# Kernel optimization log

Measured on AMD Instinct MI355X. Metric: run time of the kernel, lower is better.

Reference implementation:

```python
import jax
import jax.numpy as jnp
import numpy as np
from jax import lax

IOU_THRESH = 0.5
TOP, LEFT, BOTTOM, RIGHT = 0, 1, 2, 3


def setup_inputs() -> dict:
    key = jax.random.key(0)
    k1, k2, k3, k4, k5 = jax.random.split(key, 5)
    B, N, C = 4, 3000, 21
    # plausible boxes in (top, left, bottom, right) with positive height/width
    tl = jax.random.uniform(k1, (B, N, 2), dtype=jnp.float32) * 800.0
    wh = jax.random.uniform(k2, (B, N, 2), dtype=jnp.float32) * 200.0 + 1.0
    nms_reg = jnp.concatenate([tl, tl + wh], axis=2)
    nms_cls = jax.random.normal(k3, (B, N, 1), dtype=jnp.float32)
    rcnn_reg = jax.random.normal(k4, (B, N, 4), dtype=jnp.float32) * 2.0
    rcnn_cls = jax.random.normal(k5, (B, N, C), dtype=jnp.float32)
    return {"nms_reg": nms_reg, "nms_cls": nms_cls,
            "rcnn_reg": rcnn_reg, "rcnn_cls": rcnn_cls, "reduction": 16}


def _pairwise_iou(boxes):
    # boxes: [N, 4] in (top, left, bottom, right). IoU is invariant to the
    # (x, y) axis permutation the original applies before torchvision.nms.
    t, l, b, r = boxes[:, 0], boxes[:, 1], boxes[:, 2], boxes[:, 3]
    area = jnp.maximum(b - t, 0.0) * jnp.maximum(r - l, 0.0)  # [N]
    ih = jnp.maximum(jnp.minimum(b[:, None], b[None, :]) - jnp.maximum(t[:, None], t[None, :]), 0.0)
    iw = jnp.maximum(jnp.minimum(r[:, None], r[None, :]) - jnp.maximum(l[:, None], l[None, :]), 0.0)
    inter = ih * iw  # [N, N]
    union = area[:, None] + area[None, :] - inter
    return inter / jnp.maximum(union, 1e-9)


def _nms_keep(iou, scores):
    # Greedy NMS over one class. iou: [N, N]; scores: [N] (-inf = not this class).
    # Matches torchvision.ops.nms: suppress boxes with IoU > threshold.
    N = scores.shape[0]
    idx = jnp.arange(N)

    def step(state, _):
        rem, keep = state
        i = jnp.argmax(rem)
        valid = rem[i] > -jnp.inf
        keep = keep.at[i].set(valid)
        suppress = (iou[i] > IOU_THRESH) | (idx == i)
        rem = jnp.where(valid & suppress, -jnp.inf, rem)
        return (rem, keep), None

    (_, keep), _ = lax.scan(step, (scores, jnp.zeros(N, dtype=bool)), None, length=N)
    return keep


def reference(nms_reg, nms_cls, rcnn_reg, rcnn_cls, reduction):
    red = jnp.float32(reduction)
    # round top/left down, bottom/right up on the feature grid, back to pixels
    nms_reg_rounded = jnp.concatenate(
        [jnp.floor(nms_reg[:, :, :2] * red), jnp.ceil(nms_reg[:, :, 2:] * red)],
        axis=2) / red
    # rcnn_reg[:, :, c] += nms_reg_rounded[:, :, c] for all 4 coords
    boxes = rcnn_reg + nms_reg_rounded  # [B, N, 4]
    probs = jax.nn.softmax(rcnn_cls, axis=2)  # [B, N, C]
    nms_cls_sig = jax.nn.sigmoid(nms_cls)

    amax = jnp.argmax(probs, axis=2)  # [B, N]
    C = probs.shape[2]
    class_ids = jnp.arange(1, C)  # skip background class 0
    # per-class masked scores: [B, C-1, N]
    cls_scores = jnp.transpose(probs, (0, 2, 1))[:, 1:, :]
    scores = jnp.where(amax[:, None, :] == class_ids[None, :, None],
                       cls_scores, -jnp.inf)

    iou = jax.vmap(_pairwise_iou)(boxes)  # [B, N, N] (shared across classes)
    keep_per_class = jax.vmap(lambda io, sc: jax.vmap(lambda s: _nms_keep(io, s))(sc))(iou, scores)  # [B, C-1, N]
    keep = jnp.any(keep_per_class, axis=1)  # [B, N]; argmax classes are disjoint

    return (nms_reg_rounded, nms_cls_sig, boxes, probs, keep)
```

## Files before the change

### kernel.cpp

```cpp
#include <hip/hip_runtime.h>
#include <cfloat>
#include <climits>

#define B 4
#define N 3000
#define C 21
#define SORT_N 256
#define WORDS 4
#define NMS_BLOCKS (B * (C - 1))
#define PW_BLOCKS 12
#define TPB 1024


__device__ __forceinline__ int softmax_am(const float* __restrict__ lg,
                                          float* __restrict__ pmax_out,
                                          float* __restrict__ pstore) {
    float m = lg[0];
    #pragma unroll
    for (int c = 1; c < C; ++c) m = fmaxf(m, lg[c]);
    float p[C];
    float sum = 0.0f;
    #pragma unroll
    for (int c = 0; c < C; ++c) {
        p[c] = expf(__fsub_rn(lg[c], m));
        sum = __fadd_rn(sum, p[c]);
    }
    float best = -1.0f; int bc = 0;
    #pragma unroll
    for (int c = 0; c < C; ++c) {
        float pc = __fdiv_rn(p[c], sum);
        if (pstore) pstore[c] = pc;
        if (pc > best) { best = pc; bc = c; }
    }
    *pmax_out = best;
    return bc;
}

__device__ __forceinline__ void make_boxes(float4 nr, float4 rr, float red,
                                           float4* rounded, float4* box) {
    float r0 = floorf(__fmul_rn(nr.x, red)) / red;
    float r1 = floorf(__fmul_rn(nr.y, red)) / red;
    float r2 = ceilf (__fmul_rn(nr.z, red)) / red;
    float r3 = ceilf (__fmul_rn(nr.w, red)) / red;
    *rounded = make_float4(r0, r1, r2, r3);
    *box = make_float4(__fadd_rn(rr.x, r0), __fadd_rn(rr.y, r1),
                       __fadd_rn(rr.z, r2), __fadd_rn(rr.w, r3));
}

__global__ __launch_bounds__(TPB) void fused_kernel(
    const float* __restrict__ nms_reg,
    const float* __restrict__ nms_cls,
    const float* __restrict__ rcnn_reg,
    const float* __restrict__ rcnn_cls,
    const int* __restrict__ red_p,
    float* __restrict__ out)
{
    const int tid = threadIdx.x;

    float* out_round = out;
    float* out_sig   = out + B * N * 4;
    float* out_boxes = out + B * N * 5;
    float* out_probs = out + B * N * 9;
    float* out_keep  = out + B * N * 30;

    if (blockIdx.x >= NMS_BLOCKS) {
        const int bn = (blockIdx.x - NMS_BLOCKS) * TPB + tid;
        if (bn >= B * N) return;

        float red = (float)(*red_p);

        float4 nr = ((const float4*)nms_reg)[bn];
        float4 rr = ((const float4*)rcnn_reg)[bn];
        float4 rounded, box;
        make_boxes(nr, rr, red, &rounded, &box);
        ((float4*)out_round)[bn] = rounded;
        ((float4*)out_boxes)[bn] = box;

        float x = nms_cls[bn];
        float s;
        if (x >= 0.0f) s = 1.0f / (1.0f + expf(-x));
        else { float e = expf(x); s = e / (1.0f + e); }
        out_sig[bn] = s;

        float pm;
        int am = softmax_am(rcnn_cls + (size_t)bn * C, &pm, out_probs + (size_t)bn * C);

        if (am == 0) out_keep[bn] = 0.0f;
        return;
    }

    const int b = blockIdx.x / (C - 1);
    const int c = blockIdx.x % (C - 1) + 1;
    const int lane = tid & 63;

    __shared__ int   gid[SORT_N];
    __shared__ float gsc[SORT_N];
    __shared__ int   rnk[SORT_N];
    __shared__ int   sid[SORT_N];
    __shared__ float bt[SORT_N], bl[SORT_N], bb[SORT_N], br_[SORT_N], ar[SORT_N];
    __shared__ __align__(16) unsigned long long msk[SORT_N][WORDS];
    __shared__ unsigned long long aout[WORDS];
    __shared__ int mcount;

    if (tid == 0) mcount = 0;
    if (tid < SORT_N) rnk[tid] = 0;
    __syncthreads();

    #pragma unroll
    for (int chunk = 0; chunk < 3; ++chunk) {
        int n = chunk * TPB + tid;
        bool match = false;
        float pm = 0.0f;
        if (n < N) {
            int am = softmax_am(rcnn_cls + (size_t)(b * N + n) * C, &pm, nullptr);
            match = (am == c);
        }
        unsigned long long mb = __ballot(match);
        int base = 0;
        if (lane == 0 && mb) base = atomicAdd(&mcount, __popcll(mb));
        base = __shfl(base, 0);
        if (match) {
            int pos = base + __popcll(mb & ((1ull << lane) - 1ull));
            if (pos < SORT_N) { gid[pos] = n; gsc[pos] = pm; }
        }
    }
    __syncthreads();
    const int M = min(mcount, SORT_N);

    {
        int e = tid & 255, q = tid >> 8;
        if (e < M) {
            float mys = gsc[e]; int myi = gid[e];
            int j0 = q * 64, j1 = min(j0 + 64, M);
            int partial = 0;
            for (int j = j0; j < j1; ++j) {
                float sj = gsc[j]; int ij = gid[j];
                partial += ((sj > mys) || (sj == mys && ij < myi)) ? 1 : 0;
            }
            if (partial) atomicAdd(&rnk[e], partial);
        }
    }
    __syncthreads();

    if (tid < M) {
        float red = (float)(*red_p);
        int n = gid[tid];
        int rank = rnk[tid];
        float4 nr = ((const float4*)nms_reg)[b * N + n];
        float4 rr = ((const float4*)rcnn_reg)[b * N + n];
        float4 rounded, box;
        make_boxes(nr, rr, red, &rounded, &box);
        sid[rank] = n;
        bt[rank] = box.x; bl[rank] = box.y; bb[rank] = box.z; br_[rank] = box.w;
        ar[rank] = __fmul_rn(fmaxf(__fsub_rn(box.z, box.x), 0.0f),
                             fmaxf(__fsub_rn(box.w, box.y), 0.0f));
    }
    __syncthreads();

    {
        int g = tid >> 8;
        int j = tid & 255;
        int w = (tid >> 6) & 3;
        float jt = 0.f, jl = 0.f, jb = 0.f, jr = 0.f, ja = 0.f;
        if (j < M) { jt = bt[j]; jl = bl[j]; jb = bb[j]; jr = br_[j]; ja = ar[j]; }
        int r0 = g * 64, r1 = min(r0 + 64, M);
        const double THR = 0.5 + 0x1p-25;
        for (int r = r0; r < r1; ++r) {
            float rt = bt[r], rl = bl[r], rb = bb[r], rr2 = br_[r], ra = ar[r];
            bool supp = false;
            if (j > r && j < M) {
                float ih = fmaxf(__fsub_rn(fminf(rb, jb), fmaxf(rt, jt)), 0.0f);
                float iw = fmaxf(__fsub_rn(fminf(rr2, jr), fmaxf(rl, jl)), 0.0f);
                float inter = __fmul_rn(ih, iw);
                float uni = __fsub_rn(__fadd_rn(ra, ja), inter);
                float den = fmaxf(uni, 1e-9f);
                supp = ((double)inter > (double)den * THR);
            }
            unsigned long long wm = __ballot(supp);
            if (lane == 0) msk[r][w] = wm;
        }
    }
    __syncthreads();

    if (tid < 64) {
        auto onesk = [](int k) -> unsigned long long {
            return k <= 0 ? 0ull : (k >= 64 ? ~0ull : ((1ull << k) - 1ull));
        };
        unsigned long long a0 = onesk(M), a1 = onesk(M - 64), a2 = onesk(M - 128), a3 = onesk(M - 192);
        {
            int e = min(64, M);
            #pragma unroll 4
            for (int i = 0; i < e; ++i) {
                unsigned long long sel = 0ull - ((a0 >> i) & 1ull);
                a0 &= ~(msk[i][0] & sel);
                a1 &= ~(msk[i][1] & sel);
                a2 &= ~(msk[i][2] & sel);
                a3 &= ~(msk[i][3] & sel);
            }
        }
        {
            int e = min(128, M);
            #pragma unroll 4
            for (int i = 64; i < e; ++i) {
                unsigned long long sel = 0ull - ((a1 >> (i - 64)) & 1ull);
                a1 &= ~(msk[i][1] & sel);
                a2 &= ~(msk[i][2] & sel);
                a3 &= ~(msk[i][3] & sel);
            }
        }
        {
            int e = min(192, M);
            #pragma unroll 4
            for (int i = 128; i < e; ++i) {
                unsigned long long sel = 0ull - ((a2 >> (i - 128)) & 1ull);
                a2 &= ~(msk[i][2] & sel);
                a3 &= ~(msk[i][3] & sel);
            }
        }
        {
            int e = min(256, M);
            #pragma unroll 4
            for (int i = 192; i < e; ++i) {
                unsigned long long sel = 0ull - ((a3 >> (i - 192)) & 1ull);
                a3 &= ~(msk[i][3] & sel);
            }
        }
        if (lane == 0) { aout[0] = a0; aout[1] = a1; aout[2] = a2; aout[3] = a3; }
    }
    __syncthreads();

    if (tid < M) {
        unsigned long long aw = aout[tid >> 6];
        bool kept = (aw >> (tid & 63)) & 1ull;
        int n = sid[tid];
        out_keep[b * N + n] = (kept && n != 0) ? 1.0f : 0.0f;
    }
}

extern "C" void kernel_launch(void* const* d_in, const int* in_sizes, int n_in,
                              void* d_out, int out_size, void* d_ws, size_t ws_size,
                              hipStream_t stream) {
    const float* nms_reg  = (const float*)d_in[0];
    const float* nms_cls  = (const float*)d_in[1];
    const float* rcnn_reg = (const float*)d_in[2];
    const float* rcnn_cls = (const float*)d_in[3];
    const int*   red_p    = (const int*)d_in[4];
    float* out = (float*)d_out;

    dim3 grid(NMS_BLOCKS + PW_BLOCKS);
    fused_kernel<<<grid, TPB, 0, stream>>>(nms_reg, nms_cls, rcnn_reg, rcnn_cls, red_p, out);
}
```

Measured before the change: 102.1 us.

## Stage class logits through shared memory tiles with coalesced loads in NMS blocks

Each NMS block now copies the batch's rcnn_cls logits into a padded shared-memory tile with coalesced global reads, then computes softmax and argmax from shared memory instead of making strided per-thread row reads. The argmax is taken on unnormalised exponentials and the max probability becomes 1/sum, with an exact-division fallback when several exponentials are close to the maximum. The staging buffer is reused for the box arrays and suppression mask to keep the shared-memory footprint down. In exchange, only 500 of 1024 threads do compute per tile, and the extra barriers serialise load and compute across six tiles.

```diff
diff --git a/kernel.cpp b/kernel.cpp
--- a/kernel.cpp
+++ b/kernel.cpp
@@ -10,31 +10,10 @@
 #define NMS_BLOCKS (B * (C - 1))
 #define PW_BLOCKS 12
 #define TPB 1024
-
-
-__device__ __forceinline__ int softmax_am(const float* __restrict__ lg,
-                                          float* __restrict__ pmax_out,
-                                          float* __restrict__ pstore) {
-    float m = lg[0];
-    #pragma unroll
-    for (int c = 1; c < C; ++c) m = fmaxf(m, lg[c]);
-    float p[C];
-    float sum = 0.0f;
-    #pragma unroll
-    for (int c = 0; c < C; ++c) {
-        p[c] = expf(__fsub_rn(lg[c], m));
-        sum = __fadd_rn(sum, p[c]);
-    }
-    float best = -1.0f; int bc = 0;
-    #pragma unroll
-    for (int c = 0; c < C; ++c) {
-        float pc = __fdiv_rn(p[c], sum);
-        if (pstore) pstore[c] = pc;
-        if (pc > best) { best = pc; bc = c; }
-    }
-    *pmax_out = best;
-    return bc;
-}
+#define TILE_ROWS 500
+#define NTILES 6
+#define ROW_PITCH 23
+
 
 __device__ __forceinline__ void make_boxes(float4 nr, float4 rr, float red,
                                            float4* rounded, float4* box) {
@@ -82,38 +61,95 @@
         else { float e = expf(x); s = e / (1.0f + e); }
         out_sig[bn] = s;
 
-        float pm;
-        int am = softmax_am(rcnn_cls + (size_t)bn * C, &pm, out_probs + (size_t)bn * C);
-
+        const float* lg = rcnn_cls + (size_t)bn * C;
+        float m = lg[0];
+        #pragma unroll
+        for (int cc = 1; cc < C; ++cc) m = fmaxf(m, lg[cc]);
+        float p[C];
+        float sum = 0.0f;
+        #pragma unroll
+        for (int cc = 0; cc < C; ++cc) {
+            p[cc] = expf(__fsub_rn(lg[cc], m));
+            sum = __fadd_rn(sum, p[cc]);
+        }
+        float* po = out_probs + (size_t)bn * C;
+        float best = -1.0f; int am = 0;
+        #pragma unroll
+        for (int cc = 0; cc < C; ++cc) {
+            float pc = __fdiv_rn(p[cc], sum);
+            po[cc] = pc;
+            if (pc > best) { best = pc; am = cc; }
+        }
         if (am == 0) out_keep[bn] = 0.0f;
         return;
     }
 
     const int b = blockIdx.x / (C - 1);
-    const int c = blockIdx.x % (C - 1) + 1;
+    const int cblk = blockIdx.x % (C - 1) + 1;
     const int lane = tid & 63;
 
     __shared__ int   gid[SORT_N];
     __shared__ float gsc[SORT_N];
     __shared__ int   rnk[SORT_N];
     __shared__ int   sid[SORT_N];
-    __shared__ float bt[SORT_N], bl[SORT_N], bb[SORT_N], br_[SORT_N], ar[SORT_N];
-    __shared__ __align__(16) unsigned long long msk[SORT_N][WORDS];
     __shared__ unsigned long long aout[WORDS];
     __shared__ int mcount;
+    __shared__ __align__(16) char ubuf[TILE_ROWS * ROW_PITCH * 4];
+    float* stage = (float*)ubuf;
+    float* bt  = (float*)ubuf;
+    float* bl  = bt + SORT_N;
+    float* bb  = bl + SORT_N;
+    float* br_ = bb + SORT_N;
+    float* ar  = br_ + SORT_N;
+    unsigned long long* msk = (unsigned long long*)(ubuf + 5 * SORT_N * 4);
 
     if (tid == 0) mcount = 0;
     if (tid < SORT_N) rnk[tid] = 0;
     __syncthreads();
 
-    #pragma unroll
-    for (int chunk = 0; chunk < 3; ++chunk) {
-        int n = chunk * TPB + tid;
-        bool match = false;
-        float pm = 0.0f;
-        if (n < N) {
-            int am = softmax_am(rcnn_cls + (size_t)(b * N + n) * C, &pm, nullptr);
-            match = (am == c);
+    for (int t = 0; t < NTILES; ++t) {
+        const float* gsrc = rcnn_cls + ((size_t)b * N + t * TILE_ROWS) * C;
+        for (int w = tid; w < TILE_ROWS * C; w += TPB) {
+            int r = w / C;
+            int col = w - r * C;
+            stage[r * ROW_PITCH + col] = gsrc[w];
+        }
+        __syncthreads();
+
+        bool match = false; float score = 0.0f; int nrow = 0;
+        if (tid < TILE_ROWS) {
+            const float* row = stage + tid * ROW_PITCH;
+            float lgv[C];
+            #pragma unroll
+            for (int cc = 0; cc < C; ++cc) lgv[cc] = row[cc];
+            float m = lgv[0];
+            #pragma unroll
+            for (int cc = 1; cc < C; ++cc) m = fmaxf(m, lgv[cc]);
+            float p[C];
+            float sum = 0.0f;
+            float pm = -1.0f; int am = 0;
+            #pragma unroll
+            for (int cc = 0; cc < C; ++cc) {
+                p[cc] = expf(__fsub_rn(lgv[cc], m));
+                sum = __fadd_rn(sum, p[cc]);
+                if (p[cc] > pm) { pm = p[cc]; am = cc; }
+            }
+            int near = 0;
+            #pragma unroll
+            for (int cc = 0; cc < C; ++cc) near += (p[cc] >= 0.9999995f) ? 1 : 0;
+            if (near > 1) {
+                float best = -1.0f; am = 0;
+                #pragma unroll
+                for (int cc = 0; cc < C; ++cc) {
+                    float pc = __fdiv_rn(p[cc], sum);
+                    if (pc > best) { best = pc; am = cc; }
+                }
+                score = best;
+            } else {
+                score = __fdiv_rn(1.0f, sum);
+            }
+            match = (am == cblk);
+            nrow = t * TILE_ROWS + tid;
         }
         unsigned long long mb = __ballot(match);
         int base = 0;
@@ -121,10 +157,10 @@
         base = __shfl(base, 0);
         if (match) {
             int pos = base + __popcll(mb & ((1ull << lane) - 1ull));
-            if (pos < SORT_N) { gid[pos] = n; gsc[pos] = pm; }
-        }
-    }
-    __syncthreads();
+            if (pos < SORT_N) { gid[pos] = nrow; gsc[pos] = score; }
+        }
+        __syncthreads();
+    }
     const int M = min(mcount, SORT_N);
 
     {
@@ -177,7 +213,7 @@
                 supp = ((double)inter > (double)den * THR);
             }
             unsigned long long wm = __ballot(supp);
-            if (lane == 0) msk[r][w] = wm;
+            if (lane == 0) msk[(r << 2) | w] = wm;
         }
     }
     __syncthreads();
@@ -192,10 +228,10 @@
             #pragma unroll 4
             for (int i = 0; i < e; ++i) {
                 unsigned long long sel = 0ull - ((a0 >> i) & 1ull);
-                a0 &= ~(msk[i][0] & sel);
-                a1 &= ~(msk[i][1] & sel);
-                a2 &= ~(msk[i][2] & sel);
-                a3 &= ~(msk[i][3] & sel);
+                a0 &= ~(msk[(i << 2) | 0] & sel);
+                a1 &= ~(msk[(i << 2) | 1] & sel);
+                a2 &= ~(msk[(i << 2) | 2] & sel);
+                a3 &= ~(msk[(i << 2) | 3] & sel);
             }
         }
         {
@@ -203,9 +239,9 @@
             #pragma unroll 4
             for (int i = 64; i < e; ++i) {
                 unsigned long long sel = 0ull - ((a1 >> (i - 64)) & 1ull);
-                a1 &= ~(msk[i][1] & sel);
-                a2 &= ~(msk[i][2] & sel);
-                a3 &= ~(msk[i][3] & sel);
+                a1 &= ~(msk[(i << 2) | 1] & sel);
+                a2 &= ~(msk[(i << 2) | 2] & sel);
+                a3 &= ~(msk[(i << 2) | 3] & sel);
             }
         }
         {
@@ -213,8 +249,8 @@
             #pragma unroll 4
             for (int i = 128; i < e; ++i) {
                 unsigned long long sel = 0ull - ((a2 >> (i - 128)) & 1ull);
-                a2 &= ~(msk[i][2] & sel);
-                a3 &= ~(msk[i][3] & sel);
+                a2 &= ~(msk[(i << 2) | 2] & sel);
+                a3 &= ~(msk[(i << 2) | 3] & sel);
             }
         }
         {
@@ -222,7 +258,7 @@
             #pragma unroll 4
             for (int i = 192; i < e; ++i) {
                 unsigned long long sel = 0ull - ((a3 >> (i - 192)) & 1ull);
-                a3 &= ~(msk[i][3] & sel);
+                a3 &= ~(msk[(i << 2) | 3] & sel);
             }
         }
         if (lane == 0) { aout[0] = a0; aout[1] = a1; aout[2] = a2; aout[3] = a3; }
```

Result: slower. 116.8 us (+14.3%).

## Stage softmax rows through LDS for coalesced loads/stores across more blocks

Applied to the files above, without the earlier changes.

The pointwise blocks now load each group of 69 rows of logits into shared memory with coalesced reads, run the softmax per row from LDS, write probabilities back to LDS, then store them coalesced to global memory. The pointwise work is also spread over 176 blocks instead of 12. The goal is to remove strided per-thread 21-float global accesses and to improve parallelism. In exchange, only 69 of 1024 threads do the per-row compute, and the blocks pay for extra barriers and LDS traffic.

```diff
diff --git a/kernel.cpp b/kernel.cpp
--- a/kernel.cpp
+++ b/kernel.cpp
@@ -8,8 +8,10 @@
 #define SORT_N 256
 #define WORDS 4
 #define NMS_BLOCKS (B * (C - 1))
-#define PW_BLOCKS 12
+#define PW_BLOCKS 176
+#define PW_ROWS 69
 #define TPB 1024
+#define PITCH 23
 
 
 __device__ __forceinline__ int softmax_am(const float* __restrict__ lg,
@@ -64,28 +66,53 @@
     float* out_keep  = out + B * N * 30;
 
     if (blockIdx.x >= NMS_BLOCKS) {
-        const int bn = (blockIdx.x - NMS_BLOCKS) * TPB + tid;
-        if (bn >= B * N) return;
-
-        float red = (float)(*red_p);
-
-        float4 nr = ((const float4*)nms_reg)[bn];
-        float4 rr = ((const float4*)rcnn_reg)[bn];
-        float4 rounded, box;
-        make_boxes(nr, rr, red, &rounded, &box);
-        ((float4*)out_round)[bn] = rounded;
-        ((float4*)out_boxes)[bn] = box;
-
-        float x = nms_cls[bn];
-        float s;
-        if (x >= 0.0f) s = 1.0f / (1.0f + expf(-x));
-        else { float e = expf(x); s = e / (1.0f + e); }
-        out_sig[bn] = s;
-
-        float pm;
-        int am = softmax_am(rcnn_cls + (size_t)bn * C, &pm, out_probs + (size_t)bn * C);
-
-        if (am == 0) out_keep[bn] = 0.0f;
+        __shared__ float stage[PW_ROWS * PITCH];
+        const int pwid = blockIdx.x - NMS_BLOCKS;
+        const int row0 = pwid * PW_ROWS;
+        const int nrows = min(PW_ROWS, B * N - row0);
+        if (nrows <= 0) return;
+        const int cnt = nrows * C;
+
+        const float* gl = rcnn_cls + (size_t)row0 * C;
+        for (int w = tid; w < cnt; w += TPB) {
+            int r = w / C;
+            stage[r * PITCH + (w - r * C)] = gl[w];
+        }
+        __syncthreads();
+
+        if (tid < nrows) {
+            const int bn = row0 + tid;
+            float red = (float)(*red_p);
+
+            float4 nr = ((const float4*)nms_reg)[bn];
+            float4 rr = ((const float4*)rcnn_reg)[bn];
+            float4 rounded, box;
+            make_boxes(nr, rr, red, &rounded, &box);
+            ((float4*)out_round)[bn] = rounded;
+            ((float4*)out_boxes)[bn] = box;
+
+            float x = nms_cls[bn];
+            float s;
+            if (x >= 0.0f) s = 1.0f / (1.0f + expf(-x));
+            else { float e = expf(x); s = e / (1.0f + e); }
+            out_sig[bn] = s;
+
+            float* row = stage + tid * PITCH;
+            float lgv[C];
+            #pragma unroll
+            for (int cc = 0; cc < C; ++cc) lgv[cc] = row[cc];
+            float pm;
+            int am = softmax_am(lgv, &pm, row);
+
+            if (am == 0) out_keep[bn] = 0.0f;
+        }
+        __syncthreads();
+
+        float* po = out_probs + (size_t)row0 * C;
+        for (int w = tid; w < cnt; w += TPB) {
+            int r = w / C;
+            po[w] = stage[r * PITCH + (w - r * C)];
+        }
         return;
     }
 
```

After: 103.1 us (median of 2 runs). No clear change (+0.9%).
